# Optimization experiments

Hardware: AMD Instinct MI355X
Metric: run time of the kernel (lower is better)

Reference implementation:

```python
import jax, jax.numpy as jnp
import numpy as np

B, T, V, H, F = 128, 20, 10000, 512, 49


def _uniform(key, shape, fan):
    s = 1.0 / np.sqrt(fan)
    return jax.random.uniform(key, shape, jnp.float32, -s, s)


def setup_inputs() -> dict:
    key = jax.random.key(0)
    ks = jax.random.split(key, 16)
    return {
        "caption_inputs": jax.random.randint(ks[0], (B, T), 0, V),
        "global_features": jax.random.normal(ks[1], (B, H), jnp.float32),
        "area_features": jax.random.normal(ks[2], (B, H, F), jnp.float32),
        "h0": jnp.zeros((B, H), jnp.float32),
        "c0": jnp.zeros((B, H), jnp.float32),
        # learned params
        "embedding": jax.random.normal(ks[3], (V, H), jnp.float32),
        "W_ih": _uniform(ks[4], (2 * H, 4 * H), H),   # LSTMCell input weights (x @ W_ih)
        "W_hh": _uniform(ks[5], (H, 4 * H), H),
        "b_ih": _uniform(ks[6], (4 * H,), H),
        "b_hh": _uniform(ks[7], (4 * H,), H),
        "Wv": _uniform(ks[8], (H, H), H),             # attention comp_visual
        "Wh": _uniform(ks[9], (H, H), H),             # attention comp_hidden
        "wo": _uniform(ks[10], (H,), H),              # attention output_layer
        "W_out": _uniform(ks[11], (2 * H, V), 2 * H), # decoder output layer
        "b_out": _uniform(ks[12], (V,), 2 * H),
    }


def reference(caption_inputs, global_features, area_features, h0, c0,
              embedding, W_ih, W_hh, b_ih, b_hh, Wv, Wh, wo, W_out, b_out):
    # Precompute attention visual projection (time-invariant): [B,F,H]
    feat = jnp.swapaxes(area_features, 1, 2)          # [B,F,H]
    Vproj = jnp.einsum('bfh,hk->bfk', feat, Wv)       # [B,F,H]
    bias = b_ih + b_hh

    def step(carry, tok):
        h, c = carry
        emb = embedding[tok]                           # [B,H]
        x = jnp.concatenate([emb, global_features], axis=1)   # [B,2H]
        gates = x @ W_ih + h @ W_hh + bias             # [B,4H]
        i, f, g, o = jnp.split(gates, 4, axis=1)
        c = jax.nn.sigmoid(f) * c + jax.nn.sigmoid(i) * jnp.tanh(g)
        h = jax.nn.sigmoid(o) * jnp.tanh(c)
        # spatial attention over F locations
        z = jnp.tanh(Vproj + (h @ Wh)[:, None, :])     # [B,F,H]
        scores = jnp.einsum('bfh,h->bf', z, wo)        # [B,F]
        alpha = jax.nn.softmax(scores, axis=1)
        attended = jnp.einsum('bhf,bf->bh', area_features, alpha)  # [B,H]
        out = jnp.concatenate([h, attended], axis=1) @ W_out + b_out  # [B,V]
        return (h, c), out

    (_, _), outs = jax.lax.scan(step, (h0, c0), caption_inputs.T)  # [T,B,V]
    return jnp.swapaxes(outs, 0, 1)                    # [B,T,V]
```

## Files before the change

kernel.cpp:

```cpp
#include <hip/hip_runtime.h>

#define B_ 128
#define T_ 20
#define V_ 10000
#define H_ 512
#define F_ 49
#define NBLK_ 128

typedef unsigned short u16;
typedef __attribute__((ext_vector_type(8))) short short8;
typedef __attribute__((ext_vector_type(4))) float floatx4;

#define GLOBAL_AS __attribute__((address_space(1)))
#define LDS_AS    __attribute__((address_space(3)))

__device__ inline void load_lds16(const void* g, void* l) {
    __builtin_amdgcn_global_load_lds((const GLOBAL_AS void*)g, (LDS_AS void*)l, 16, 0, 0);
}

__device__ inline u16 f2b(float v) {
    unsigned u = __builtin_bit_cast(unsigned, v);
    unsigned rounding = 0x7FFFu + ((u >> 16) & 1u);
    return (u16)((u + rounding) >> 16);
}
__device__ inline float b2f(u16 h) {
    unsigned u = ((unsigned)h) << 16;
    return __builtin_bit_cast(float, u);
}
__device__ inline float fast_tanh(float x) {
    return 1.f - 2.f / (__expf(2.f * x) + 1.f);
}
__device__ inline float sigm(float x) { return 1.f / (1.f + __expf(-x)); }

__global__ __launch_bounds__(256) void transpose_cvt(const float* __restrict__ src,
                                                     u16* __restrict__ dst, int K, int N) {
    __shared__ float tile[32][33];
    int n0 = blockIdx.x * 32, k0 = blockIdx.y * 32;
    int tx = threadIdx.x, ty = threadIdx.y;
    #pragma unroll
    for (int i = 0; i < 32; i += 8) {
        int k = k0 + ty + i, n = n0 + tx;
        tile[ty + i][tx] = (k < K && n < N) ? src[(size_t)k * N + n] : 0.f;
    }
    __syncthreads();
    #pragma unroll
    for (int i = 0; i < 32; i += 8) {
        int n = n0 + ty + i, k = k0 + tx;
        if (n < N && k < K) dst[(size_t)n * K + k] = f2b(tile[tx][ty + i]);
    }
}

__global__ __launch_bounds__(256) void build_x(const int* __restrict__ cap,
                                               const float* __restrict__ emb,
                                               const float* __restrict__ gf,
                                               u16* __restrict__ X) {
    int r = blockIdx.x;
    int t = r / B_, b = r % B_;
    int tok = cap[b * T_ + t];
    for (int col = threadIdx.x; col < 2 * H_; col += 256) {
        float v = (col < H_) ? emb[(size_t)tok * H_ + col] : gf[(size_t)b * H_ + (col - H_)];
        X[(size_t)r * (2 * H_) + col] = f2b(v);
    }
}

__global__ __launch_bounds__(256) void feat_cvt(const float* __restrict__ area,
                                                u16* __restrict__ feat) {
    int idx = blockIdx.x * 256 + threadIdx.x;
    if (idx >= B_ * F_ * H_) return;
    int h = idx & (H_ - 1);
    int bf_ = idx >> 9;
    int f = bf_ % F_, b = bf_ / F_;
    feat[idx] = f2b(area[((size_t)b * H_ + h) * F_ + f]);
}

__global__ __launch_bounds__(256) void init_hc(const float* __restrict__ h0,
                                               u16* __restrict__ Hall, int* __restrict__ bar) {
    int i = blockIdx.x * 256 + threadIdx.x;
    if (i < B_ * H_) Hall[i] = f2b(h0[i]);
    if (i < 256) bar[i] = 0;
}

__device__ inline void grid_sync_mg(int* base, int ep) {
    __syncthreads();
    if (threadIdx.x == 0) {
        int old = __hip_atomic_fetch_add(&base[0], 1, __ATOMIC_ACQ_REL, __HIP_MEMORY_SCOPE_AGENT);
        if (old == ep * 32 - 1)
            __hip_atomic_store(&base[32], ep, __ATOMIC_RELEASE, __HIP_MEMORY_SCOPE_AGENT);
        while (__hip_atomic_load(&base[32], __ATOMIC_RELAXED, __HIP_MEMORY_SCOPE_AGENT) < ep)
            __builtin_amdgcn_s_sleep(2);
        (void)__hip_atomic_load(&base[32], __ATOMIC_ACQUIRE, __HIP_MEMORY_SCOPE_AGENT);
    }
    __syncthreads();
}

__global__ __launch_bounds__(256, 1) void decode_loop(
        const u16* __restrict__ WhhT, const float* __restrict__ Xin,
        const float* __restrict__ c0, u16* __restrict__ Hall,
        int* __restrict__ bar) {

    __shared__ __align__(16) u16 Whs[64 * 512];
    __shared__ __align__(16) u16 hstage[32 * 512];
    __shared__ float gl[4 * 32 * 16];
    __shared__ float csh[32 * 16];

    const int tid = threadIdx.x;
    const int wave = tid >> 6, lane = tid & 63;
    const int lm = lane & 15, q = lane >> 4;
    const int bid = blockIdx.x;
    const int jg = bid >> 2, mg = bid & 3;
    int* mybar = bar + mg * 64;

    #pragma unroll
    for (int i = 0; i < 16; ++i) {
        int row = i * 4 + wave;
        int g = row >> 4, lr = row & 15;
        int grow = g * H_ + jg * 16 + lr;
        load_lds16(WhhT + (size_t)grow * H_ + (size_t)(lane ^ (row & 7)) * 8,
                   (char*)Whs + row * 1024);
    }
    #pragma unroll
    for (int ii = 0; ii < 2; ++ii) {
        int idx = tid + ii * 256;
        int lb = idx >> 4, jj = idx & 15;
        csh[idx] = c0[(size_t)(mg * 32 + lb) * H_ + jg * 16 + jj];
    }

    for (int t = 0; t < T_; ++t) {
        const u16* hprev = Hall + (size_t)t * B_ * H_;
        u16* hnext = Hall + (size_t)(t + 1) * B_ * H_;

        #pragma unroll
        for (int it = 0; it < 8; ++it) {
            int row = it * 4 + wave;
            load_lds16(hprev + (size_t)(mg * 32 + row) * H_ + (size_t)(lane ^ (row & 7)) * 8,
                       (char*)hstage + row * 1024);
        }
        __syncthreads();

        floatx4 acc0 = {0.f, 0.f, 0.f, 0.f}, acc1 = {0.f, 0.f, 0.f, 0.f};
        #pragma unroll
        for (int kt = 0; kt < 16; ++kt) {
            int ch = kt * 4 + q;
            short8 a0 = *(const short8*)&hstage[(lm << 9) + ((ch ^ (lm & 7)) << 3)];
            short8 a1 = *(const short8*)&hstage[((16 + lm) << 9) + ((ch ^ (lm & 7)) << 3)];
            short8 bb = *(const short8*)&Whs[((wave * 16 + lm) << 9) + ((ch ^ (lm & 7)) << 3)];
            acc0 = __builtin_amdgcn_mfma_f32_16x16x32_bf16(a0, bb, acc0, 0, 0, 0);
            acc1 = __builtin_amdgcn_mfma_f32_16x16x32_bf16(a1, bb, acc1, 0, 0, 0);
        }
        #pragma unroll
        for (int r = 0; r < 4; ++r) {
            gl[wave * 512 + (q * 4 + r) * 16 + lm] = acc0[r];
            gl[wave * 512 + (16 + q * 4 + r) * 16 + lm] = acc1[r];
        }
        __syncthreads();

        #pragma unroll
        for (int ii = 0; ii < 2; ++ii) {
            int idx = tid + ii * 256;
            int lb = idx >> 4, jj = idx & 15;
            int grow = mg * 32 + lb, j = jg * 16 + jj;
            const float* xt = Xin + ((size_t)t * B_ + grow) * (4 * H_);
            float gi = gl[0 * 512 + lb * 16 + jj] + xt[j];
            float gf = gl[1 * 512 + lb * 16 + jj] + xt[H_ + j];
            float gg = gl[2 * 512 + lb * 16 + jj] + xt[2 * H_ + j];
            float go = gl[3 * 512 + lb * 16 + jj] + xt[3 * H_ + j];
            float cn = sigm(gf) * csh[idx] + sigm(gi) * fast_tanh(gg);
            csh[idx] = cn;
            hnext[(size_t)grow * H_ + j] = f2b(sigm(go) * fast_tanh(cn));
        }

        grid_sync_mg(mybar, t + 1);
    }
}

__global__ __launch_bounds__(256) void attn_post(
        const float* __restrict__ ahbuf, const u16* __restrict__ Vprojb,
        const u16* __restrict__ feat, const float* __restrict__ wo,
        const u16* __restrict__ Hall, u16* __restrict__ Hcat) {
    __shared__ __align__(16) u16 Vsh[F_ * H_];
    __shared__ __align__(16) u16 fsh[F_ * H_];
    __shared__ float ash[H_];
    __shared__ float wosh[H_];
    __shared__ float sc[64];

    const int tid = threadIdx.x;
    const int wave = tid >> 6, lane = tid & 63;
    const int b = blockIdx.x >> 1, th = blockIdx.x & 1;

    const short8* vsrc = (const short8*)(Vprojb + (size_t)b * F_ * H_);
    const short8* fsrc = (const short8*)(feat + (size_t)b * F_ * H_);
    for (int i = tid; i < F_ * H_ / 8; i += 256) {
        ((short8*)Vsh)[i] = vsrc[i];
        ((short8*)fsh)[i] = fsrc[i];
    }
    for (int i = tid; i < H_; i += 256) wosh[i] = wo[i];
    __syncthreads();

    for (int t = th * (T_ / 2); t < (th + 1) * (T_ / 2); ++t) {
        for (int i = tid; i < H_; i += 256)
            ash[i] = ahbuf[((size_t)t * B_ + b) * H_ + i];
        __syncthreads();

        for (int f = wave; f < F_; f += 4) {
            short8 vv = *(const short8*)&Vsh[f * H_ + lane * 8];
            float s = 0.f;
            #pragma unroll
            for (int e = 0; e < 8; ++e) {
                int h = lane * 8 + e;
                s += wosh[h] * fast_tanh(b2f((u16)vv[e]) + ash[h]);
            }
            #pragma unroll
            for (int off = 32; off; off >>= 1) s += __shfl_xor(s, off);
            if (lane == 0) sc[f] = s;
        }
        __syncthreads();

        if (tid < 64) {
            float v = (tid < F_) ? sc[tid] : -1e30f;
            float m = v;
            #pragma unroll
            for (int off = 32; off; off >>= 1) m = fmaxf(m, __shfl_xor(m, off));
            float e = (tid < F_) ? __expf(v - m) : 0.f;
            float sum = e;
            #pragma unroll
            for (int off = 32; off; off >>= 1) sum += __shfl_xor(sum, off);
            if (tid < F_) sc[tid] = e / sum;
        }
        __syncthreads();

        const size_t rowo = ((size_t)b * T_ + t) * (2 * H_);
        const short8* hrow = (const short8*)(Hall + ((size_t)(t + 1) * B_ + b) * H_);
        for (int i = tid; i < H_ / 8; i += 256)
            ((short8*)(Hcat + rowo))[i] = hrow[i];
        for (int h = tid; h < H_; h += 256) {
            float acc = 0.f;
            #pragma unroll
            for (int f = 0; f < F_; ++f) acc += b2f(fsh[f * H_ + h]) * sc[f];
            Hcat[rowo + H_ + h] = f2b(acc);
        }
        __syncthreads();
    }
}

template <int WRITE_BF16>
__global__ __launch_bounds__(256) void gemm2(const u16* __restrict__ A, int lda,
                                             const u16* __restrict__ Bt, int ldb,
                                             void* __restrict__ Cout, int ldc,
                                             const float* __restrict__ bias1,
                                             const float* __restrict__ bias2,
                                             int M, int N, int K) {
    __shared__ __align__(16) u16 As[128 * 32];
    __shared__ __align__(16) u16 Bs[128 * 32];
    const int tid = threadIdx.x, wave = tid >> 6, lane = tid & 63;
    const int wr = wave >> 1, wc = wave & 1;
    const int lm = lane & 15, q = lane >> 4;
    const int m0 = blockIdx.x * 128, n0 = blockIdx.y * 128;

    const int off = wave * 1024 + lane * 16;
    const int r0 = off >> 6;
    const int c0 = (off & 63) >> 1;

    const u16* gA0 = A + (size_t)(m0 + r0) * lda + c0;
    const u16* gA1 = A + (size_t)(m0 + r0 + 64) * lda + c0;
    int nb0 = n0 + r0;      if (nb0 > N - 1) nb0 = N - 1;
    int nb1 = n0 + r0 + 64; if (nb1 > N - 1) nb1 = N - 1;
    const u16* gB0 = Bt + (size_t)nb0 * ldb + c0;
    const u16* gB1 = Bt + (size_t)nb1 * ldb + c0;
    char* lA0 = (char*)As + wave * 1024;
    char* lA1 = (char*)As + 4096 + wave * 1024;
    char* lB0 = (char*)Bs + wave * 1024;
    char* lB1 = (char*)Bs + 4096 + wave * 1024;

    floatx4 acc[4][4];
    #pragma unroll
    for (int i = 0; i < 4; ++i)
        #pragma unroll
        for (int j = 0; j < 4; ++j) acc[i][j] = floatx4{0.f, 0.f, 0.f, 0.f};

    const int nkt = K >> 5;
    for (int kt = 0; kt < nkt; ++kt) {
        const int ko = kt * 32;
        load_lds16(gA0 + ko, lA0);
        load_lds16(gA1 + ko, lA1);
        load_lds16(gB0 + ko, lB0);
        load_lds16(gB1 + ko, lB1);
        __syncthreads();
        short8 af[4], bf[4];
        #pragma unroll
        for (int i = 0; i < 4; ++i)
            af[i] = *(const short8*)&As[(wr * 64 + i * 16 + lm) * 32 + q * 8];
        #pragma unroll
        for (int j = 0; j < 4; ++j)
            bf[j] = *(const short8*)&Bs[(wc * 64 + j * 16 + lm) * 32 + q * 8];
        #pragma unroll
        for (int i = 0; i < 4; ++i)
            #pragma unroll
            for (int j = 0; j < 4; ++j)
                acc[i][j] = __builtin_amdgcn_mfma_f32_16x16x32_bf16(af[i], bf[j], acc[i][j], 0, 0, 0);
        __syncthreads();
    }

    #pragma unroll
    for (int i = 0; i < 4; ++i) {
        const int row = m0 + wr * 64 + i * 16 + q * 4;
        #pragma unroll
        for (int j = 0; j < 4; ++j) {
            const int col = n0 + wc * 64 + j * 16 + lm;
            if (col < N) {
                #pragma unroll
                for (int r = 0; r < 4; ++r) {
                    float v = acc[i][j][r];
                    if (bias1) v += bias1[col];
                    if (bias2) v += bias2[col];
                    if (WRITE_BF16) ((u16*)Cout)[(size_t)(row + r) * ldc + col] = f2b(v);
                    else            ((float*)Cout)[(size_t)(row + r) * ldc + col] = v;
                }
            }
        }
    }
}

extern "C" void kernel_launch(void* const* d_in, const int* in_sizes, int n_in,
                              void* d_out, int out_size, void* d_ws, size_t ws_size,
                              hipStream_t stream) {
    const int*   cap   = (const int*)d_in[0];
    const float* gf    = (const float*)d_in[1];
    const float* area  = (const float*)d_in[2];
    const float* h0    = (const float*)d_in[3];
    const float* c0    = (const float*)d_in[4];
    const float* emb   = (const float*)d_in[5];
    const float* W_ih  = (const float*)d_in[6];
    const float* W_hh  = (const float*)d_in[7];
    const float* b_ih  = (const float*)d_in[8];
    const float* b_hh  = (const float*)d_in[9];
    const float* Wv    = (const float*)d_in[10];
    const float* Wh    = (const float*)d_in[11];
    const float* wo    = (const float*)d_in[12];
    const float* W_out = (const float*)d_in[13];
    const float* b_out = (const float*)d_in[14];
    float* out = (float*)d_out;

    char* p = (char*)d_ws;
    auto alloc = [&](size_t bytes) {
        char* q = p;
        p += (bytes + 255) & ~(size_t)255;
        return q;
    };
    u16*   X      = (u16*)alloc((size_t)T_ * B_ * 2 * H_ * 2);
    u16*   WihT   = (u16*)alloc((size_t)4 * H_ * 2 * H_ * 2);
    u16*   WhhT   = (u16*)alloc((size_t)4 * H_ * H_ * 2);
    u16*   WvT    = (u16*)alloc((size_t)H_ * H_ * 2);
    u16*   WhT    = (u16*)alloc((size_t)H_ * H_ * 2);
    u16*   WoutT  = (u16*)alloc((size_t)V_ * 2 * H_ * 2);
    u16*   feat   = (u16*)alloc((size_t)B_ * F_ * H_ * 2);
    float* Xin    = (float*)alloc((size_t)T_ * B_ * 4 * H_ * 4);
    u16*   Vprojb = (u16*)alloc((size_t)B_ * F_ * H_ * 2);
    float* ahbuf  = (float*)alloc((size_t)T_ * B_ * H_ * 4);
    u16*   Hall   = (u16*)alloc((size_t)(T_ + 1) * B_ * H_ * 2);
    int*   bar    = (int*)alloc(1024);
    u16*   Hcat   = (u16*)alloc((size_t)B_ * T_ * 2 * H_ * 2);

    dim3 tb(32, 8);
    transpose_cvt<<<dim3(4 * H_ / 32, 2 * H_ / 32), tb, 0, stream>>>(W_ih, WihT, 2 * H_, 4 * H_);
    transpose_cvt<<<dim3(4 * H_ / 32, H_ / 32), tb, 0, stream>>>(W_hh, WhhT, H_, 4 * H_);
    transpose_cvt<<<dim3(H_ / 32, H_ / 32), tb, 0, stream>>>(Wv, WvT, H_, H_);
    transpose_cvt<<<dim3(H_ / 32, H_ / 32), tb, 0, stream>>>(Wh, WhT, H_, H_);
    transpose_cvt<<<dim3((V_ + 31) / 32, 2 * H_ / 32), tb, 0, stream>>>(W_out, WoutT, 2 * H_, V_);
    build_x<<<T_ * B_, 256, 0, stream>>>(cap, emb, gf, X);
    feat_cvt<<<(B_ * F_ * H_ + 255) / 256, 256, 0, stream>>>(area, feat);
    init_hc<<<(B_ * H_ + 255) / 256, 256, 0, stream>>>(h0, Hall, bar);

    gemm2<0><<<dim3(T_ * B_ / 128, 4 * H_ / 128), 256, 0, stream>>>(
        X, 2 * H_, WihT, 2 * H_, Xin, 4 * H_, b_ih, b_hh, T_ * B_, 4 * H_, 2 * H_);
    gemm2<1><<<dim3(B_ * F_ / 128, H_ / 128), 256, 0, stream>>>(
        feat, H_, WvT, H_, Vprojb, H_, nullptr, nullptr, B_ * F_, H_, H_);

    decode_loop<<<NBLK_, 256, 0, stream>>>(WhhT, Xin, c0, Hall, bar);

    gemm2<0><<<dim3(T_ * B_ / 128, H_ / 128), 256, 0, stream>>>(
        Hall + (size_t)B_ * H_, H_, WhT, H_, ahbuf, H_, nullptr, nullptr, T_ * B_, H_, H_);

    attn_post<<<2 * B_, 256, 0, stream>>>(ahbuf, Vprojb, feat, wo, Hall, Hcat);

    gemm2<0><<<dim3(T_ * B_ / 128, (V_ + 127) / 128), 256, 0, stream>>>(
        Hcat, 2 * H_, WoutT, 2 * H_, out, V_, b_out, nullptr, T_ * B_, V_, 2 * H_);
}
```

Before: 652.6 us.

## Merge preprocessing kernels into one launch, pair GEMMs, prefetch Xin in decode loop

After: 601.3 us. -7.9%, faster.

```diff
diff --git a/kernel.cpp b/kernel.cpp
--- a/kernel.cpp
+++ b/kernel.cpp
@@ -32,11 +32,10 @@
 }
 __device__ inline float sigm(float x) { return 1.f / (1.f + __expf(-x)); }
 
-__global__ __launch_bounds__(256) void transpose_cvt(const float* __restrict__ src,
-                                                     u16* __restrict__ dst, int K, int N) {
-    __shared__ float tile[32][33];
-    int n0 = blockIdx.x * 32, k0 = blockIdx.y * 32;
-    int tx = threadIdx.x, ty = threadIdx.y;
+__device__ __forceinline__ void tr32(const float* __restrict__ src, u16* __restrict__ dst,
+                                     int K, int N, int bx, int by, int tx, int ty,
+                                     float (*tile)[33]) {
+    int n0 = bx * 32, k0 = by * 32;
     #pragma unroll
     for (int i = 0; i < 32; i += 8) {
         int k = k0 + ty + i, n = n0 + tx;
@@ -50,34 +49,53 @@
     }
 }
 
-__global__ __launch_bounds__(256) void build_x(const int* __restrict__ cap,
-                                               const float* __restrict__ emb,
-                                               const float* __restrict__ gf,
-                                               u16* __restrict__ X) {
-    int r = blockIdx.x;
-    int t = r / B_, b = r % B_;
-    int tok = cap[b * T_ + t];
-    for (int col = threadIdx.x; col < 2 * H_; col += 256) {
-        float v = (col < H_) ? emb[(size_t)tok * H_ + col] : gf[(size_t)b * H_ + (col - H_)];
-        X[(size_t)r * (2 * H_) + col] = f2b(v);
-    }
-}
-
-__global__ __launch_bounds__(256) void feat_cvt(const float* __restrict__ area,
-                                                u16* __restrict__ feat) {
-    int idx = blockIdx.x * 256 + threadIdx.x;
-    if (idx >= B_ * F_ * H_) return;
-    int h = idx & (H_ - 1);
-    int bf_ = idx >> 9;
-    int f = bf_ % F_, b = bf_ / F_;
-    feat[idx] = f2b(area[((size_t)b * H_ + h) * F_ + f]);
-}
-
-__global__ __launch_bounds__(256) void init_hc(const float* __restrict__ h0,
-                                               u16* __restrict__ Hall, int* __restrict__ bar) {
-    int i = blockIdx.x * 256 + threadIdx.x;
-    if (i < B_ * H_) Hall[i] = f2b(h0[i]);
-    if (i < 256) bar[i] = 0;
+__global__ __launch_bounds__(256) void preamble(
+        const float* __restrict__ W_ih, const float* __restrict__ W_hh,
+        const float* __restrict__ Wv, const float* __restrict__ Wh,
+        const float* __restrict__ W_out, const int* __restrict__ cap,
+        const float* __restrict__ emb, const float* __restrict__ gf,
+        const float* __restrict__ area, const float* __restrict__ h0,
+        u16* __restrict__ WihT, u16* __restrict__ WhhT, u16* __restrict__ WvT,
+        u16* __restrict__ WhT, u16* __restrict__ WoutT, u16* __restrict__ X,
+        u16* __restrict__ feat, u16* __restrict__ Hall, int* __restrict__ bar) {
+    __shared__ float tile[32][33];
+    const int bid = blockIdx.x, tid = threadIdx.x;
+    const int tx = tid & 31, ty = tid >> 5;
+
+    if (bid < 2048) {
+        int r = bid;                 tr32(W_ih, WihT, 1024, 2048, r % 64, r / 64, tx, ty, tile);
+    } else if (bid < 3072) {
+        int r = bid - 2048;          tr32(W_hh, WhhT, 512, 2048, r % 64, r / 64, tx, ty, tile);
+    } else if (bid < 3328) {
+        int r = bid - 3072;          tr32(Wv, WvT, 512, 512, r % 16, r / 16, tx, ty, tile);
+    } else if (bid < 3584) {
+        int r = bid - 3328;          tr32(Wh, WhT, 512, 512, r % 16, r / 16, tx, ty, tile);
+    } else if (bid < 13600) {
+        int r = bid - 3584;          tr32(W_out, WoutT, 1024, 10000, r % 313, r / 313, tx, ty, tile);
+    } else if (bid < 16160) {
+        int r = bid - 13600;
+        int t = r / B_, b = r % B_;
+        int tok = cap[b * T_ + t];
+        for (int col = tid; col < 2 * H_; col += 256) {
+            float v = (col < H_) ? emb[(size_t)tok * H_ + col] : gf[(size_t)b * H_ + (col - H_)];
+            X[(size_t)r * (2 * H_) + col] = f2b(v);
+        }
+    } else if (bid < 19296) {
+        int r = bid - 16160;
+        #pragma unroll
+        for (int k = 0; k < 4; ++k) {
+            int idx = r * 1024 + k * 256 + tid;
+            int h = idx & (H_ - 1);
+            int bf_ = idx >> 9;
+            int f = bf_ % F_, b = bf_ / F_;
+            feat[idx] = f2b(area[((size_t)b * H_ + h) * F_ + f]);
+        }
+    } else {
+        int r = bid - 19296;
+        int i = r * 256 + tid;
+        Hall[i] = f2b(h0[i]);
+        if (r == 0) bar[tid] = 0;
+    }
 }
 
 __device__ inline void grid_sync_mg(int* base, int ep) {
@@ -110,19 +128,28 @@
     const int jg = bid >> 2, mg = bid & 3;
     int* mybar = bar + mg * 64;
 
+    const int lb0 = tid >> 4, jj = tid & 15;
+    const int lb1 = lb0 + 16;
+    const int grow0 = mg * 32 + lb0, grow1 = mg * 32 + lb1;
+    const int j = jg * 16 + jj;
+
     #pragma unroll
     for (int i = 0; i < 16; ++i) {
         int row = i * 4 + wave;
         int g = row >> 4, lr = row & 15;
-        int grow = g * H_ + jg * 16 + lr;
-        load_lds16(WhhT + (size_t)grow * H_ + (size_t)(lane ^ (row & 7)) * 8,
+        int grr = g * H_ + jg * 16 + lr;
+        load_lds16(WhhT + (size_t)grr * H_ + (size_t)(lane ^ (row & 7)) * 8,
                    (char*)Whs + row * 1024);
     }
-    #pragma unroll
-    for (int ii = 0; ii < 2; ++ii) {
-        int idx = tid + ii * 256;
-        int lb = idx >> 4, jj = idx & 15;
-        csh[idx] = c0[(size_t)(mg * 32 + lb) * H_ + jg * 16 + jj];
+    csh[tid] = c0[(size_t)grow0 * H_ + j];
+    csh[tid + 256] = c0[(size_t)grow1 * H_ + j];
+
+    float xf[8];
+    {
+        const float* x0 = Xin + (size_t)grow0 * (4 * H_);
+        const float* x1 = Xin + (size_t)grow1 * (4 * H_);
+        xf[0] = x0[j]; xf[1] = x0[H_ + j]; xf[2] = x0[2 * H_ + j]; xf[3] = x0[3 * H_ + j];
+        xf[4] = x1[j]; xf[5] = x1[H_ + j]; xf[6] = x1[2 * H_ + j]; xf[7] = x1[3 * H_ + j];
     }
 
     for (int t = 0; t < T_; ++t) {
@@ -154,22 +181,36 @@
         }
         __syncthreads();
 
-        #pragma unroll
-        for (int ii = 0; ii < 2; ++ii) {
-            int idx = tid + ii * 256;
-            int lb = idx >> 4, jj = idx & 15;
-            int grow = mg * 32 + lb, j = jg * 16 + jj;
-            const float* xt = Xin + ((size_t)t * B_ + grow) * (4 * H_);
-            float gi = gl[0 * 512 + lb * 16 + jj] + xt[j];
-            float gf = gl[1 * 512 + lb * 16 + jj] + xt[H_ + j];
-            float gg = gl[2 * 512 + lb * 16 + jj] + xt[2 * H_ + j];
-            float go = gl[3 * 512 + lb * 16 + jj] + xt[3 * H_ + j];
-            float cn = sigm(gf) * csh[idx] + sigm(gi) * fast_tanh(gg);
-            csh[idx] = cn;
-            hnext[(size_t)grow * H_ + j] = f2b(sigm(go) * fast_tanh(cn));
-        }
-
-        grid_sync_mg(mybar, t + 1);
+        float xc[8];
+        #pragma unroll
+        for (int i = 0; i < 8; ++i) xc[i] = xf[i];
+        if (t + 1 < T_) {
+            const float* x0 = Xin + ((size_t)(t + 1) * B_ + grow0) * (4 * H_);
+            const float* x1 = Xin + ((size_t)(t + 1) * B_ + grow1) * (4 * H_);
+            xf[0] = x0[j]; xf[1] = x0[H_ + j]; xf[2] = x0[2 * H_ + j]; xf[3] = x0[3 * H_ + j];
+            xf[4] = x1[j]; xf[5] = x1[H_ + j]; xf[6] = x1[2 * H_ + j]; xf[7] = x1[3 * H_ + j];
+        }
+
+        {
+            float gi = gl[0 * 512 + lb0 * 16 + jj] + xc[0];
+            float gf = gl[1 * 512 + lb0 * 16 + jj] + xc[1];
+            float gg = gl[2 * 512 + lb0 * 16 + jj] + xc[2];
+            float go = gl[3 * 512 + lb0 * 16 + jj] + xc[3];
+            float cn = sigm(gf) * csh[tid] + sigm(gi) * fast_tanh(gg);
+            csh[tid] = cn;
+            hnext[(size_t)grow0 * H_ + j] = f2b(sigm(go) * fast_tanh(cn));
+        }
+        {
+            float gi = gl[0 * 512 + lb1 * 16 + jj] + xc[4];
+            float gf = gl[1 * 512 + lb1 * 16 + jj] + xc[5];
+            float gg = gl[2 * 512 + lb1 * 16 + jj] + xc[6];
+            float go = gl[3 * 512 + lb1 * 16 + jj] + xc[7];
+            float cn = sigm(gf) * csh[tid + 256] + sigm(gi) * fast_tanh(gg);
+            csh[tid + 256] = cn;
+            hnext[(size_t)grow1 * H_ + j] = f2b(sigm(go) * fast_tanh(cn));
+        }
+
+        if (t + 1 < T_) grid_sync_mg(mybar, t + 1);
     }
 }
 
@@ -243,18 +284,15 @@
 }
 
 template <int WRITE_BF16>
-__global__ __launch_bounds__(256) void gemm2(const u16* __restrict__ A, int lda,
-                                             const u16* __restrict__ Bt, int ldb,
-                                             void* __restrict__ Cout, int ldc,
-                                             const float* __restrict__ bias1,
-                                             const float* __restrict__ bias2,
-                                             int M, int N, int K) {
-    __shared__ __align__(16) u16 As[128 * 32];
-    __shared__ __align__(16) u16 Bs[128 * 32];
+__device__ __forceinline__ void gemm2_body(
+        const u16* __restrict__ A, int lda, const u16* __restrict__ Bt, int ldb,
+        void* __restrict__ Cout, int ldc, const float* __restrict__ bias1,
+        const float* __restrict__ bias2, int M, int N, int K, int bx, int by,
+        u16* As, u16* Bs) {
     const int tid = threadIdx.x, wave = tid >> 6, lane = tid & 63;
     const int wr = wave >> 1, wc = wave & 1;
     const int lm = lane & 15, q = lane >> 4;
-    const int m0 = blockIdx.x * 128, n0 = blockIdx.y * 128;
+    const int m0 = bx * 128, n0 = by * 128;
 
     const int off = wave * 1024 + lane * 16;
     const int r0 = off >> 6;
@@ -275,7 +313,7 @@
     #pragma unroll
     for (int i = 0; i < 4; ++i)
         #pragma unroll
-        for (int j = 0; j < 4; ++j) acc[i][j] = floatx4{0.f, 0.f, 0.f, 0.f};
+        for (int jq = 0; jq < 4; ++jq) acc[i][jq] = floatx4{0.f, 0.f, 0.f, 0.f};
 
     const int nkt = K >> 5;
     for (int kt = 0; kt < nkt; ++kt) {
@@ -290,13 +328,13 @@
         for (int i = 0; i < 4; ++i)
             af[i] = *(const short8*)&As[(wr * 64 + i * 16 + lm) * 32 + q * 8];
         #pragma unroll
-        for (int j = 0; j < 4; ++j)
-            bf[j] = *(const short8*)&Bs[(wc * 64 + j * 16 + lm) * 32 + q * 8];
+        for (int jq = 0; jq < 4; ++jq)
+            bf[jq] = *(const short8*)&Bs[(wc * 64 + jq * 16 + lm) * 32 + q * 8];
         #pragma unroll
         for (int i = 0; i < 4; ++i)
             #pragma unroll
-            for (int j = 0; j < 4; ++j)
-                acc[i][j] = __builtin_amdgcn_mfma_f32_16x16x32_bf16(af[i], bf[j], acc[i][j], 0, 0, 0);
+            for (int jq = 0; jq < 4; ++jq)
+                acc[i][jq] = __builtin_amdgcn_mfma_f32_16x16x32_bf16(af[i], bf[jq], acc[i][jq], 0, 0, 0);
         __syncthreads();
     }
 
@@ -304,12 +342,12 @@
     for (int i = 0; i < 4; ++i) {
         const int row = m0 + wr * 64 + i * 16 + q * 4;
         #pragma unroll
-        for (int j = 0; j < 4; ++j) {
-            const int col = n0 + wc * 64 + j * 16 + lm;
+        for (int jq = 0; jq < 4; ++jq) {
+            const int col = n0 + wc * 64 + jq * 16 + lm;
             if (col < N) {
                 #pragma unroll
                 for (int r = 0; r < 4; ++r) {
-                    float v = acc[i][j][r];
+                    float v = acc[i][jq][r];
                     if (bias1) v += bias1[col];
                     if (bias2) v += bias2[col];
                     if (WRITE_BF16) ((u16*)Cout)[(size_t)(row + r) * ldc + col] = f2b(v);
@@ -317,6 +355,37 @@
                 }
             }
         }
+    }
+}
+
+template <int WRITE_BF16>
+__global__ __launch_bounds__(256) void gemm2(const u16* __restrict__ A, int lda,
+                                             const u16* __restrict__ Bt, int ldb,
+                                             void* __restrict__ Cout, int ldc,
+                                             const float* __restrict__ bias1,
+                                             const float* __restrict__ bias2,
+                                             int M, int N, int K) {
+    __shared__ __align__(16) u16 As[128 * 32];
+    __shared__ __align__(16) u16 Bs[128 * 32];
+    gemm2_body<WRITE_BF16>(A, lda, Bt, ldb, Cout, ldc, bias1, bias2, M, N, K,
+                           blockIdx.x, blockIdx.y, As, Bs);
+}
+
+__global__ __launch_bounds__(256) void gemm_pair(
+        const u16* __restrict__ X, const u16* __restrict__ WihT,
+        float* __restrict__ Xin, const float* __restrict__ b_ih,
+        const float* __restrict__ b_hh, const u16* __restrict__ feat,
+        const u16* __restrict__ WvT, u16* __restrict__ Vprojb) {
+    __shared__ __align__(16) u16 As[128 * 32];
+    __shared__ __align__(16) u16 Bs[128 * 32];
+    int bid = blockIdx.x;
+    if (bid < 320) {
+        gemm2_body<0>(X, 2 * H_, WihT, 2 * H_, Xin, 4 * H_, b_ih, b_hh,
+                      T_ * B_, 4 * H_, 2 * H_, bid % 20, bid / 20, As, Bs);
+    } else {
+        int r = bid - 320;
+        gemm2_body<1>(feat, H_, WvT, H_, Vprojb, H_, nullptr, nullptr,
+                      B_ * F_, H_, H_, r % 49, r / 49, As, Bs);
     }
 }
 
@@ -360,20 +429,11 @@
     int*   bar    = (int*)alloc(1024);
     u16*   Hcat   = (u16*)alloc((size_t)B_ * T_ * 2 * H_ * 2);
 
-    dim3 tb(32, 8);
-    transpose_cvt<<<dim3(4 * H_ / 32, 2 * H_ / 32), tb, 0, stream>>>(W_ih, WihT, 2 * H_, 4 * H_);
-    transpose_cvt<<<dim3(4 * H_ / 32, H_ / 32), tb, 0, stream>>>(W_hh, WhhT, H_, 4 * H_);
-    transpose_cvt<<<dim3(H_ / 32, H_ / 32), tb, 0, stream>>>(Wv, WvT, H_, H_);
-    transpose_cvt<<<dim3(H_ / 32, H_ / 32), tb, 0, stream>>>(Wh, WhT, H_, H_);
-    transpose_cvt<<<dim3((V_ + 31) / 32, 2 * H_ / 32), tb, 0, stream>>>(W_out, WoutT, 2 * H_, V_);
-    build_x<<<T_ * B_, 256, 0, stream>>>(cap, emb, gf, X);
-    feat_cvt<<<(B_ * F_ * H_ + 255) / 256, 256, 0, stream>>>(area, feat);
-    init_hc<<<(B_ * H_ + 255) / 256, 256, 0, stream>>>(h0, Hall, bar);
-
-    gemm2<0><<<dim3(T_ * B_ / 128, 4 * H_ / 128), 256, 0, stream>>>(
-        X, 2 * H_, WihT, 2 * H_, Xin, 4 * H_, b_ih, b_hh, T_ * B_, 4 * H_, 2 * H_);
-    gemm2<1><<<dim3(B_ * F_ / 128, H_ / 128), 256, 0, stream>>>(
-        feat, H_, WvT, H_, Vprojb, H_, nullptr, nullptr, B_ * F_, H_, H_);
+    preamble<<<19552, 256, 0, stream>>>(W_ih, W_hh, Wv, Wh, W_out, cap, emb, gf,
+                                        area, h0, WihT, WhhT, WvT, WhT, WoutT,
+                                        X, feat, Hall, bar);
+
+    gemm_pair<<<516, 256, 0, stream>>>(X, WihT, Xin, b_ih, b_hh, feat, WvT, Vprojb);
 
     decode_loop<<<NBLK_, 256, 0, stream>>>(WhhT, Xin, c0, Hall, bar);
 
```
